# Kernel tuning notes

Hardware: AMD Instinct MI355X
Metric: run time of the kernel (lower is better)

The kernel has to match this reference:

```python
import jax, jax.numpy as jnp
import numpy as np

B, T, D, H, O = 256, 512, 128, 256, 128

def setup_inputs() -> dict:
    key = jax.random.key(0)
    ks = jax.random.split(key, 7)
    s = lambda k, shape, fan: jax.random.normal(k, shape, dtype=jnp.float32) / np.sqrt(fan)
    return {
        "x": jax.random.normal(ks[0], (B, T, D), dtype=jnp.float32),
        "W_hx_w": s(ks[1], (H, D), D),
        "W_hx_b": jnp.zeros((H,), jnp.float32),
        "W_hh_w": s(ks[2], (H, H), H),
        "W_hh_b": jnp.zeros((H,), jnp.float32),
        "W_ph_w": s(ks[3], (O, H), H),
        "W_ph_b": jnp.zeros((O,), jnp.float32),
    }

def reference(x, W_hx_w, W_hx_b, W_hh_w, W_hh_b, W_ph_w, W_ph_b):
    # Precompute the input projection for all timesteps in one batched GEMM.
    xW = jnp.einsum('btd,hd->bth', x, W_hx_w) + W_hx_b  # [B,T,H]
    h0 = jnp.zeros((x.shape[0], W_hh_w.shape[0]), x.dtype)

    def step(h, xw_t):
        h_new = jnp.tanh(xw_t + h @ W_hh_w.T + W_hh_b)
        return h_new, None

    h_T, _ = jax.lax.scan(step, h0, jnp.swapaxes(xW, 0, 1))  # scan over T
    out = h_T @ W_ph_w.T + W_ph_b  # [B,O]
    return out
```

## Files before the change

kernel.cpp:

```cpp
#include <hip/hip_runtime.h>


typedef _Float16 f16;
typedef _Float16 f16x2 __attribute__((ext_vector_type(2)));
typedef _Float16 f16x4 __attribute__((ext_vector_type(4)));
typedef _Float16 f16x8 __attribute__((ext_vector_type(8)));
typedef float f32x4 __attribute__((ext_vector_type(4)));

#define NB 256
#define NT 512
#define ND 128
#define NH 256
#define NO 128
#define R  16
#define TCH 8
#define NCH (NT / TCH)
#define STEP_F16 4096
#define WS_NEED ((size_t)16 * NT * STEP_F16 * 2)

__device__ __forceinline__ float fast_tanh(float z) {
  float e = __builtin_amdgcn_exp2f(z * 2.88539008177793f);
  float r = __builtin_amdgcn_rcpf(e + 1.0f);
  return __builtin_fmaf(-2.0f, r, 1.0f);
}

__device__ __forceinline__ f16x8 cvt8(const float* __restrict__ p) {
  f32x4 v0 = *(const f32x4*)p;
  f32x4 v1 = *(const f32x4*)(p + 4);
  f16x8 r;
  r[0] = (f16)v0.x; r[1] = (f16)v0.y; r[2] = (f16)v0.z; r[3] = (f16)v0.w;
  r[4] = (f16)v1.x; r[5] = (f16)v1.y; r[6] = (f16)v1.z; r[7] = (f16)v1.w;
  return r;
}

__device__ __forceinline__ f16x8 cvt44(const float* __restrict__ p0,
                                       const float* __restrict__ p1) {
  f32x4 a = *(const f32x4*)p0;
  f32x4 b = *(const f32x4*)p1;
  f16x8 r;
  r[0] = (f16)a.x; r[1] = (f16)a.y; r[2] = (f16)a.z; r[3] = (f16)a.w;
  r[4] = (f16)b.x; r[5] = (f16)b.y; r[6] = (f16)b.z; r[7] = (f16)b.w;
  return r;
}

__global__ __launch_bounds__(256, 2)
void xw_gemm(const float* __restrict__ x,
             const float* __restrict__ Wx, const float* __restrict__ bx,
             const float* __restrict__ bh, f16* __restrict__ ws)
{
  const int wgb = blockIdx.x & 15;
  const int c   = blockIdx.x >> 4;
  const int tid = threadIdx.x;
  const int w   = tid >> 6;
  const int l15 = tid & 15;
  const int g   = (tid >> 4) & 3;

  __shared__ alignas(16) f16 xlds[TCH * R][ND];

  f16x8 fWx[4][4];
  f32x4 bias4[4];
  #pragma unroll
  for (int ct = 0; ct < 4; ++ct) {
    const int j = w * 64 + ct * 16 + l15;
    #pragma unroll
    for (int kt = 0; kt < 4; ++kt)
      fWx[ct][kt] = cvt8(Wx + (size_t)j * ND + kt * 32 + g * 8);
    const int j0 = w * 64 + ct * 16 + g * 4;
    #pragma unroll
    for (int rg = 0; rg < 4; ++rg)
      bias4[ct][rg] = bx[j0 + rg] + bh[j0 + rg];
  }

  const int srow = tid >> 4;
  const int sq   = tid & 15;
  const float* xc = x + ((size_t)(wgb * R + srow) * NT + (size_t)c * TCH) * ND;
  #pragma unroll
  for (int jj = 0; jj < 16; ++jj) {
    const int f = (sq + jj * 16) * 4;
    f32x4 v = *(const f32x4*)(xc + f);
    const int t = f >> 7;
    const int d = f & (ND - 1);
    const int m = t * R + srow;
    f16x4 h4;
    h4[0] = (f16)v.x; h4[1] = (f16)v.y; h4[2] = (f16)v.z; h4[3] = (f16)v.w;
    *(f16x4*)((char*)&xlds[m][0] + ((2 * d) ^ ((m & 7) << 4))) = h4;
  }
  __syncthreads();

  #pragma unroll
  for (int t = 0; t < TCH; ++t) {
    f16x8 b[4];
    #pragma unroll
    for (int kt = 0; kt < 4; ++kt) {
      const int m = t * R + l15;
      b[kt] = *(const f16x8*)((char*)&xlds[m][0] +
               ((kt * 64 + g * 16) ^ ((m & 7) << 4)));
    }
    f16* wsp = ws + ((size_t)(wgb * NT + c * TCH + t)) * STEP_F16
                  + w * 1024 + g * 64 + l15 * 4;
    #pragma unroll
    for (int ct = 0; ct < 4; ++ct) {
      f32x4 ac = bias4[ct];
      #pragma unroll
      for (int kt = 0; kt < 4; ++kt)
        ac = __builtin_amdgcn_mfma_f32_16x16x32_f16(fWx[ct][kt], b[kt], ac, 0, 0, 0);
      f16x4 p;
      p[0] = (f16)ac[0]; p[1] = (f16)ac[1]; p[2] = (f16)ac[2]; p[3] = (f16)ac[3];
      *(f16x4*)(wsp + ct * 256) = p;
    }
  }
}

#define DO_STEP(CUR, ACIN, ACOUT, XWPF, XWIN, H8K, TAU)                     \
  {                                                                         \
    f16x8 bfr[7];                                                           \
    _Pragma("unroll")                                                       \
    for (int kr = 1; kr < 8; ++kr)                                          \
      bfr[kr - 1] = *(const f16x8*)((const char*)&hbuf[CUR][l15][0] +       \
                ((((w2 + kr) * 4 + g + l15) & 31) << 4));                   \
    int pf = (TAU) + 2; pf = pf < NT ? pf : NT - 1;                         \
    _Pragma("unroll")                                                       \
    for (int ct = 0; ct < 2; ++ct)                                          \
      XWPF[ct] = *(const f16x4*)(wsg + (size_t)pf * STEP_F16 + ct * 256);   \
    _Pragma("unroll")                                                       \
    for (int ct = 0; ct < 2; ++ct)                                          \
      ACIN[ct] = __builtin_amdgcn_mfma_f32_16x16x32_f16(fWh[ct][0], H8K,    \
                   ACIN[ct], 0, 0, 0);                                      \
    _Pragma("unroll")                                                       \
    for (int kr = 1; kr < 8; ++kr) {                                        \
      _Pragma("unroll")                                                     \
      for (int ct = 0; ct < 2; ++ct)                                        \
        ACIN[ct] = __builtin_amdgcn_mfma_f32_16x16x32_f16(fWh[ct][kr],      \
                     bfr[kr - 1], ACIN[ct], 0, 0, 0);                       \
    }                                                                       \
    {                                                                       \
      f16x8 h8;                                                             \
      _Pragma("unroll")                                                     \
      for (int ct = 0; ct < 2; ++ct)                                        \
        _Pragma("unroll")                                                   \
        for (int rg = 0; rg < 4; ++rg)                                      \
          h8[ct * 4 + rg] = (f16)fast_tanh(ACIN[ct][rg]);                   \
      *(f16x8*)((char*)&hbuf[(CUR) ^ 1][l15][0] +                           \
                (((w2 * 4 + g + l15) & 31) << 4)) = h8;                     \
      H8K = h8;                                                             \
    }                                                                       \
    _Pragma("unroll")                                                       \
    for (int ct = 0; ct < 2; ++ct) {                                        \
      ACOUT[ct][0] = (float)XWIN[ct][0]; ACOUT[ct][1] = (float)XWIN[ct][1]; \
      ACOUT[ct][2] = (float)XWIN[ct][2]; ACOUT[ct][3] = (float)XWIN[ct][3]; \
    }                                                                       \
    asm volatile("s_waitcnt lgkmcnt(0)\n\ts_barrier" ::: "memory");         \
    __builtin_amdgcn_sched_barrier(0);                                      \
  }

__global__ __launch_bounds__(512, 2)
void rnn_scan(const f16* __restrict__ ws,
              const float* __restrict__ Wh,
              const float* __restrict__ Wp, const float* __restrict__ bp,
              float* __restrict__ out)
{
  const int wg  = blockIdx.x;
  const int tid = threadIdx.x;
  const int w2  = tid >> 6;
  const int l15 = tid & 15;
  const int g   = (tid >> 4) & 3;

  __shared__ alignas(16) f16 hbuf[2][R][NH];

  f16x8 fWh[2][8];
  #pragma unroll
  for (int ct = 0; ct < 2; ++ct) {
    const int j = w2 * 32 + ct * 16 + l15;
    #pragma unroll
    for (int kr = 0; kr < 8; ++kr) {
      const int kta = (w2 + kr) & 7;
      fWh[ct][kr] = cvt44(Wh + (size_t)j * NH + kta * 32 + g * 4,
                          Wh + (size_t)j * NH + kta * 32 + 16 + g * 4);
    }
  }

  {
    unsigned* hz = (unsigned*)&hbuf[0][0][0];
    #pragma unroll
    for (int k = 0; k < (2 * R * NH / 2) / 512; ++k) hz[tid + k * 512] = 0u;
  }

  const f16* wsg = ws + (size_t)wg * NT * STEP_F16
                 + (size_t)(w2 * 2) * 256 + g * 64 + l15 * 4;

  f16x4 xA[2], xB[2];
  #pragma unroll
  for (int ct = 0; ct < 2; ++ct) xA[ct] = *(const f16x4*)(wsg + 0 * STEP_F16 + ct * 256);
  #pragma unroll
  for (int ct = 0; ct < 2; ++ct) xB[ct] = *(const f16x4*)(wsg + 1 * STEP_F16 + ct * 256);

  f32x4 acA[2], acB[2];
  #pragma unroll
  for (int ct = 0; ct < 2; ++ct) {
    acA[ct][0] = (float)xA[ct][0]; acA[ct][1] = (float)xA[ct][1];
    acA[ct][2] = (float)xA[ct][2]; acA[ct][3] = (float)xA[ct][3];
  }

  f16x8 h8k;
  #pragma unroll
  for (int i = 0; i < 8; ++i) h8k[i] = (f16)0.f;

  __syncthreads();

  #pragma unroll 1
  for (int tau = 0; tau < NT; tau += 2) {
    DO_STEP(0, acA, acB, xA, xB, h8k, tau);
    DO_STEP(1, acB, acA, xB, xA, h8k, tau + 1);
  }

  f16x8 bh8[8];
  #pragma unroll
  for (int kt = 0; kt < 8; ++kt)
    bh8[kt] = *(const f16x8*)((const char*)&hbuf[0][l15][0] +
              (((kt * 4 + g + l15) & 31) << 4));
  {
    const int j0 = w2 * 16 + g * 4;
    f32x4 ac = {bp[j0], bp[j0 + 1], bp[j0 + 2], bp[j0 + 3]};
    #pragma unroll
    for (int kt = 0; kt < 8; ++kt) {
      const float* wrow = Wp + (size_t)(w2 * 16 + l15) * NH;
      f16x8 afr = cvt44(wrow + kt * 32 + g * 4, wrow + kt * 32 + 16 + g * 4);
      ac = __builtin_amdgcn_mfma_f32_16x16x32_f16(afr, bh8[kt], ac, 0, 0, 0);
    }
    #pragma unroll
    for (int rg = 0; rg < 4; ++rg)
      out[(size_t)(wg * R + l15) * NO + j0 + rg] = ac[rg];
  }
}

__global__ __launch_bounds__(256, 1)
void rnn_mfma(const float* __restrict__ x,
              const float* __restrict__ Wx, const float* __restrict__ bx,
              const float* __restrict__ Wh, const float* __restrict__ bh,
              const float* __restrict__ Wp, const float* __restrict__ bp,
              float* __restrict__ out)
{
  const int wg  = blockIdx.x;
  const int tid = threadIdx.x;
  const int w   = tid >> 6;
  const int l15 = tid & 15;
  const int g   = (tid >> 4) & 3;

  __shared__ alignas(16) f16 xlds[TCH * R][ND];
  __shared__ alignas(16) f16 hbuf[2][R][NH];

  f16x8 fWh[4][8];
  #pragma unroll
  for (int ct = 0; ct < 4; ++ct) {
    const int j = w * 64 + ct * 16 + l15;
    #pragma unroll
    for (int kt = 0; kt < 8; ++kt)
      fWh[ct][kt] = cvt8(Wh + (size_t)j * NH + kt * 32 + g * 8);
  }
  f16x8 fWx[4][4];
  #pragma unroll
  for (int ct = 0; ct < 4; ++ct) {
    const int j = w * 64 + ct * 16 + l15;
    #pragma unroll
    for (int kt = 0; kt < 4; ++kt)
      fWx[ct][kt] = cvt8(Wx + (size_t)j * ND + kt * 32 + g * 8);
  }
  float bias[4];
  #pragma unroll
  for (int ct = 0; ct < 4; ++ct) {
    const int j = w * 64 + ct * 16 + l15;
    bias[ct] = bx[j] + bh[j];
  }
  {
    unsigned* hz = (unsigned*)&hbuf[0][0][0];
    #pragma unroll
    for (int k = 0; k < (R * NH / 2) / 256; ++k) hz[tid + k * 256] = 0u;
  }
  __syncthreads();

  int cur = 0;
  f16x2 xwb[TCH][4][2];
  const int srow = tid >> 4;
  const int sq   = tid & 15;
  const float* xrow = x + (size_t)(wg * R + srow) * NT * ND;

  #pragma unroll 1
  for (int c = 0; c < NCH; ++c) {
    const float* xc = xrow + (size_t)c * TCH * ND;
    #pragma unroll
    for (int jj = 0; jj < 16; ++jj) {
      const int f = (sq + jj * 16) * 4;
      f32x4 v = *(const f32x4*)(xc + f);
      const int t = f >> 7;
      const int d = f & (ND - 1);
      const int m = t * R + srow;
      f16x4 h4;
      h4[0] = (f16)v.x; h4[1] = (f16)v.y; h4[2] = (f16)v.z; h4[3] = (f16)v.w;
      *(f16x4*)((char*)&xlds[m][0] + ((2 * d) ^ ((m & 7) << 4))) = h4;
    }
    __syncthreads();

    #pragma unroll
    for (int t = 0; t < TCH; ++t) {
      f16x8 a[4];
      #pragma unroll
      for (int kt = 0; kt < 4; ++kt) {
        const int m = t * R + l15;
        a[kt] = *(const f16x8*)((char*)&xlds[m][0] +
                 ((kt * 64 + g * 16) ^ ((m & 7) << 4)));
      }
      #pragma unroll
      for (int ct = 0; ct < 4; ++ct) {
        f32x4 ac = {bias[ct], bias[ct], bias[ct], bias[ct]};
        #pragma unroll
        for (int kt = 0; kt < 4; ++kt)
          ac = __builtin_amdgcn_mfma_f32_16x16x32_f16(a[kt], fWx[ct][kt], ac, 0, 0, 0);
        f16x2 p0; p0[0] = (f16)ac[0]; p0[1] = (f16)ac[1];
        f16x2 p1; p1[0] = (f16)ac[2]; p1[1] = (f16)ac[3];
        xwb[t][ct][0] = p0;
        xwb[t][ct][1] = p1;
      }
    }

    #pragma unroll
    for (int s = 0; s < TCH; ++s) {
      f16x8 a[8];
      #pragma unroll
      for (int kt = 0; kt < 8; ++kt) {
        const int m = l15;
        a[kt] = *(const f16x8*)((char*)&hbuf[cur][m][0] +
                 ((kt * 64 + g * 16) ^ ((m & 7) << 4)));
      }
      const int nxt = cur ^ 1;
      #pragma unroll
      for (int ct = 0; ct < 4; ++ct) {
        f32x4 ac  = {(float)xwb[s][ct][0][0], (float)xwb[s][ct][0][1],
                     (float)xwb[s][ct][1][0], (float)xwb[s][ct][1][1]};
        f32x4 ac2 = {0.f, 0.f, 0.f, 0.f};
        #pragma unroll
        for (int kt = 0; kt < 4; ++kt) {
          ac  = __builtin_amdgcn_mfma_f32_16x16x32_f16(a[2*kt],     fWh[ct][2*kt],     ac,  0, 0, 0);
          ac2 = __builtin_amdgcn_mfma_f32_16x16x32_f16(a[2*kt + 1], fWh[ct][2*kt + 1], ac2, 0, 0, 0);
        }
        #pragma unroll
        for (int rg = 0; rg < 4; ++rg) {
          const float th = fast_tanh(ac[rg] + ac2[rg]);
          const int row = g * 4 + rg;
          const int col = w * 64 + ct * 16 + l15;
          *(f16*)((char*)&hbuf[nxt][row][0] +
                  ((2 * col) ^ ((row & 7) << 4))) = (f16)th;
        }
      }
      cur = nxt;
      __syncthreads();
    }
  }

  f16x8 ah[8];
  #pragma unroll
  for (int kt = 0; kt < 8; ++kt) {
    const int m = l15;
    ah[kt] = *(const f16x8*)((char*)&hbuf[cur][m][0] +
             ((kt * 64 + g * 16) ^ ((m & 7) << 4)));
  }
  #pragma unroll
  for (int ct = 0; ct < 2; ++ct) {
    const int o = w * 32 + ct * 16 + l15;
    f32x4 ac = {bp[o], bp[o], bp[o], bp[o]};
    #pragma unroll
    for (int kt = 0; kt < 8; ++kt) {
      f16x8 bfr = cvt8(Wp + (size_t)o * NH + kt * 32 + g * 8);
      ac = __builtin_amdgcn_mfma_f32_16x16x32_f16(ah[kt], bfr, ac, 0, 0, 0);
    }
    #pragma unroll
    for (int rg = 0; rg < 4; ++rg) {
      const int row = g * 4 + rg;
      out[(size_t)(wg * R + row) * NO + o] = ac[rg];
    }
  }
}

extern "C" void kernel_launch(void* const* d_in, const int* in_sizes, int n_in,
                              void* d_out, int out_size, void* d_ws, size_t ws_size,
                              hipStream_t stream) {
  const float* x   = (const float*)d_in[0];
  const float* whx = (const float*)d_in[1];
  const float* bhx = (const float*)d_in[2];
  const float* whh = (const float*)d_in[3];
  const float* bhh = (const float*)d_in[4];
  const float* wph = (const float*)d_in[5];
  const float* bph = (const float*)d_in[6];
  float* out = (float*)d_out;

  if (ws_size >= WS_NEED) {
    f16* ws = (f16*)d_ws;
    xw_gemm<<<dim3(16 * NCH), dim3(256), 0, stream>>>(x, whx, bhx, bhh, ws);
    rnn_scan<<<dim3(16), dim3(512), 0, stream>>>(ws, whh, wph, bph, out);
  } else {
    rnn_mfma<<<dim3(NB / R), dim3(256), 0, stream>>>(x, whx, bhx, whh, bhh, wph, bph, out);
  }
}
```

Baseline: 330.2 us.

## Fuse input-projection GEMM and recurrent scan into one producer/consumer kernel

Replaces the two-launch sequence (xW GEMM, then scan) with one persistent kernel. Blocks 0-15 run the recurrence, and 240 producer blocks compute the xW chunks and publish per-chunk release flags in workspace. Scan blocks spin on acquire loads before consuming each group of chunks, so the GEMM overlaps with the serial recurrence instead of running ahead of it. This adds a memset of the flags, relies on all blocks being co-resident to avoid deadlock, and the producer order must keep ahead of the consumers.

```diff
diff --git a/kernel.cpp b/kernel.cpp
--- a/kernel.cpp
+++ b/kernel.cpp
@@ -16,7 +16,10 @@
 #define TCH 8
 #define NCH (NT / TCH)
 #define STEP_F16 4096
-#define WS_NEED ((size_t)16 * NT * STEP_F16 * 2)
+#define NPROD 240
+#define NPAIR (16 * NCH)
+#define WS_XW ((size_t)16 * NT * STEP_F16 * 2)
+#define WS_FUSED (WS_XW + 4096)
 
 __device__ __forceinline__ float fast_tanh(float z) {
   float e = __builtin_amdgcn_exp2f(z * 2.88539008177793f);
@@ -41,74 +44,6 @@
   r[0] = (f16)a.x; r[1] = (f16)a.y; r[2] = (f16)a.z; r[3] = (f16)a.w;
   r[4] = (f16)b.x; r[5] = (f16)b.y; r[6] = (f16)b.z; r[7] = (f16)b.w;
   return r;
-}
-
-__global__ __launch_bounds__(256, 2)
-void xw_gemm(const float* __restrict__ x,
-             const float* __restrict__ Wx, const float* __restrict__ bx,
-             const float* __restrict__ bh, f16* __restrict__ ws)
-{
-  const int wgb = blockIdx.x & 15;
-  const int c   = blockIdx.x >> 4;
-  const int tid = threadIdx.x;
-  const int w   = tid >> 6;
-  const int l15 = tid & 15;
-  const int g   = (tid >> 4) & 3;
-
-  __shared__ alignas(16) f16 xlds[TCH * R][ND];
-
-  f16x8 fWx[4][4];
-  f32x4 bias4[4];
-  #pragma unroll
-  for (int ct = 0; ct < 4; ++ct) {
-    const int j = w * 64 + ct * 16 + l15;
-    #pragma unroll
-    for (int kt = 0; kt < 4; ++kt)
-      fWx[ct][kt] = cvt8(Wx + (size_t)j * ND + kt * 32 + g * 8);
-    const int j0 = w * 64 + ct * 16 + g * 4;
-    #pragma unroll
-    for (int rg = 0; rg < 4; ++rg)
-      bias4[ct][rg] = bx[j0 + rg] + bh[j0 + rg];
-  }
-
-  const int srow = tid >> 4;
-  const int sq   = tid & 15;
-  const float* xc = x + ((size_t)(wgb * R + srow) * NT + (size_t)c * TCH) * ND;
-  #pragma unroll
-  for (int jj = 0; jj < 16; ++jj) {
-    const int f = (sq + jj * 16) * 4;
-    f32x4 v = *(const f32x4*)(xc + f);
-    const int t = f >> 7;
-    const int d = f & (ND - 1);
-    const int m = t * R + srow;
-    f16x4 h4;
-    h4[0] = (f16)v.x; h4[1] = (f16)v.y; h4[2] = (f16)v.z; h4[3] = (f16)v.w;
-    *(f16x4*)((char*)&xlds[m][0] + ((2 * d) ^ ((m & 7) << 4))) = h4;
-  }
-  __syncthreads();
-
-  #pragma unroll
-  for (int t = 0; t < TCH; ++t) {
-    f16x8 b[4];
-    #pragma unroll
-    for (int kt = 0; kt < 4; ++kt) {
-      const int m = t * R + l15;
-      b[kt] = *(const f16x8*)((char*)&xlds[m][0] +
-               ((kt * 64 + g * 16) ^ ((m & 7) << 4)));
-    }
-    f16* wsp = ws + ((size_t)(wgb * NT + c * TCH + t)) * STEP_F16
-                  + w * 1024 + g * 64 + l15 * 4;
-    #pragma unroll
-    for (int ct = 0; ct < 4; ++ct) {
-      f32x4 ac = bias4[ct];
-      #pragma unroll
-      for (int kt = 0; kt < 4; ++kt)
-        ac = __builtin_amdgcn_mfma_f32_16x16x32_f16(fWx[ct][kt], b[kt], ac, 0, 0, 0);
-      f16x4 p;
-      p[0] = (f16)ac[0]; p[1] = (f16)ac[1]; p[2] = (f16)ac[2]; p[3] = (f16)ac[3];
-      *(f16x4*)(wsp + ct * 256) = p;
-    }
-  }
 }
 
 #define DO_STEP(CUR, ACIN, ACOUT, XWPF, XWIN, H8K, TAU)                     \
@@ -154,6 +89,245 @@
   }
 
 __global__ __launch_bounds__(512, 2)
+void rnn_fused(const float* __restrict__ x,
+               const float* __restrict__ Wx, const float* __restrict__ bx,
+               const float* __restrict__ Wh, const float* __restrict__ bh,
+               const float* __restrict__ Wp, const float* __restrict__ bp,
+               f16* __restrict__ ws, unsigned* __restrict__ flags,
+               float* __restrict__ out)
+{
+  __shared__ alignas(16) f16 smem[16384];
+  const int tid = threadIdx.x;
+  const int w2  = tid >> 6;
+  const int l15 = tid & 15;
+  const int g   = (tid >> 4) & 3;
+
+  if (blockIdx.x >= 16) {
+    f16 (*xlds)[ND] = (f16 (*)[ND])smem;
+
+    f16x8 fWx[2][4];
+    f32x4 bias2[2];
+    #pragma unroll
+    for (int ct = 0; ct < 2; ++ct) {
+      const int j = w2 * 32 + ct * 16 + l15;
+      #pragma unroll
+      for (int kt = 0; kt < 4; ++kt)
+        fWx[ct][kt] = cvt8(Wx + (size_t)j * ND + kt * 32 + g * 8);
+      const int j0 = w2 * 32 + ct * 16 + g * 4;
+      #pragma unroll
+      for (int rg = 0; rg < 4; ++rg)
+        bias2[ct][rg] = bx[j0 + rg] + bh[j0 + rg];
+    }
+
+    #pragma unroll 1
+    for (int p = blockIdx.x - 16; p < NPAIR; p += NPROD) {
+      const int s = p & 15;
+      const int c = p >> 4;
+      #pragma unroll
+      for (int jj = 0; jj < 8; ++jj) {
+        const int fi = (tid + jj * 512) * 4;
+        const int t  = fi >> 11;
+        const int rr = (fi >> 7) & 15;
+        const int d  = fi & 127;
+        f32x4 v = *(const f32x4*)(x + ((size_t)(s * R + rr) * NT
+                                     + (size_t)(c * TCH + t)) * ND + d);
+        const int m = t * R + rr;
+        f16x4 h4;
+        h4[0] = (f16)v.x; h4[1] = (f16)v.y; h4[2] = (f16)v.z; h4[3] = (f16)v.w;
+        *(f16x4*)((char*)&xlds[m][0] + ((2 * d) ^ ((m & 7) << 4))) = h4;
+      }
+      __syncthreads();
+
+      #pragma unroll
+      for (int t = 0; t < TCH; ++t) {
+        f16x8 b[4];
+        #pragma unroll
+        for (int kt = 0; kt < 4; ++kt) {
+          const int m = t * R + l15;
+          b[kt] = *(const f16x8*)((char*)&xlds[m][0] +
+                   ((kt * 64 + g * 16) ^ ((m & 7) << 4)));
+        }
+        f16* wsp = ws + ((size_t)(s * NT + c * TCH + t)) * STEP_F16
+                      + (w2 * 2) * 256 + g * 64 + l15 * 4;
+        #pragma unroll
+        for (int ct = 0; ct < 2; ++ct) {
+          f32x4 ac = bias2[ct];
+          #pragma unroll
+          for (int kt = 0; kt < 4; ++kt)
+            ac = __builtin_amdgcn_mfma_f32_16x16x32_f16(fWx[ct][kt], b[kt], ac, 0, 0, 0);
+          f16x4 pk;
+          pk[0] = (f16)ac[0]; pk[1] = (f16)ac[1];
+          pk[2] = (f16)ac[2]; pk[3] = (f16)ac[3];
+          *(f16x4*)(wsp + ct * 256) = pk;
+        }
+      }
+      __threadfence();
+      __syncthreads();
+      if (tid == 0)
+        __hip_atomic_store(&flags[p], 1u, __ATOMIC_RELEASE,
+                           __HIP_MEMORY_SCOPE_AGENT);
+    }
+    return;
+  }
+
+  const int wg = blockIdx.x;
+  f16 (*hbuf)[R][NH] = (f16 (*)[R][NH])smem;
+
+  f16x8 fWh[2][8];
+  #pragma unroll
+  for (int ct = 0; ct < 2; ++ct) {
+    const int j = w2 * 32 + ct * 16 + l15;
+    #pragma unroll
+    for (int kr = 0; kr < 8; ++kr) {
+      const int kta = (w2 + kr) & 7;
+      fWh[ct][kr] = cvt44(Wh + (size_t)j * NH + kta * 32 + g * 4,
+                          Wh + (size_t)j * NH + kta * 32 + 16 + g * 4);
+    }
+  }
+
+  {
+    unsigned* hz = (unsigned*)&hbuf[0][0][0];
+    #pragma unroll
+    for (int k = 0; k < (2 * R * NH / 2) / 512; ++k) hz[tid + k * 512] = 0u;
+  }
+
+  if (tid < 5) {
+    int cc = tid; if (cc > NCH - 1) cc = NCH - 1;
+    const int fidx = cc * 16 + wg;
+    while (__hip_atomic_load(&flags[fidx], __ATOMIC_ACQUIRE,
+                             __HIP_MEMORY_SCOPE_AGENT) == 0u)
+      __builtin_amdgcn_s_sleep(8);
+  }
+  __syncthreads();
+
+  const f16* wsg = ws + (size_t)wg * NT * STEP_F16
+                 + (size_t)(w2 * 2) * 256 + g * 64 + l15 * 4;
+
+  f16x4 xA[2], xB[2];
+  #pragma unroll
+  for (int ct = 0; ct < 2; ++ct) xA[ct] = *(const f16x4*)(wsg + 0 * STEP_F16 + ct * 256);
+  #pragma unroll
+  for (int ct = 0; ct < 2; ++ct) xB[ct] = *(const f16x4*)(wsg + 1 * STEP_F16 + ct * 256);
+
+  f32x4 acA[2], acB[2];
+  #pragma unroll
+  for (int ct = 0; ct < 2; ++ct) {
+    acA[ct][0] = (float)xA[ct][0]; acA[ct][1] = (float)xA[ct][1];
+    acA[ct][2] = (float)xA[ct][2]; acA[ct][3] = (float)xA[ct][3];
+  }
+
+  f16x8 h8k;
+  #pragma unroll
+  for (int i = 0; i < 8; ++i) h8k[i] = (f16)0.f;
+
+  #pragma unroll 1
+  for (int c4 = 0; c4 < NCH; c4 += 4) {
+    if (c4 > 0) {
+      if (tid < 4) {
+        int cc = c4 + 1 + tid; if (cc > NCH - 1) cc = NCH - 1;
+        const int fidx = cc * 16 + wg;
+        while (__hip_atomic_load(&flags[fidx], __ATOMIC_ACQUIRE,
+                                 __HIP_MEMORY_SCOPE_AGENT) == 0u)
+          __builtin_amdgcn_s_sleep(8);
+      }
+      __syncthreads();
+    }
+    #pragma unroll 1
+    for (int tau = c4 * 8; tau < c4 * 8 + 32; tau += 2) {
+      DO_STEP(0, acA, acB, xA, xB, h8k, tau);
+      DO_STEP(1, acB, acA, xB, xA, h8k, tau + 1);
+    }
+  }
+
+  f16x8 bh8[8];
+  #pragma unroll
+  for (int kt = 0; kt < 8; ++kt)
+    bh8[kt] = *(const f16x8*)((const char*)&hbuf[0][l15][0] +
+              (((kt * 4 + g + l15) & 31) << 4));
+  {
+    const int j0 = w2 * 16 + g * 4;
+    f32x4 ac = {bp[j0], bp[j0 + 1], bp[j0 + 2], bp[j0 + 3]};
+    #pragma unroll
+    for (int kt = 0; kt < 8; ++kt) {
+      const float* wrow = Wp + (size_t)(w2 * 16 + l15) * NH;
+      f16x8 afr = cvt44(wrow + kt * 32 + g * 4, wrow + kt * 32 + 16 + g * 4);
+      ac = __builtin_amdgcn_mfma_f32_16x16x32_f16(afr, bh8[kt], ac, 0, 0, 0);
+    }
+    #pragma unroll
+    for (int rg = 0; rg < 4; ++rg)
+      out[(size_t)(wg * R + l15) * NO + j0 + rg] = ac[rg];
+  }
+}
+
+__global__ __launch_bounds__(256, 2)
+void xw_gemm(const float* __restrict__ x,
+             const float* __restrict__ Wx, const float* __restrict__ bx,
+             const float* __restrict__ bh, f16* __restrict__ ws)
+{
+  const int wgb = blockIdx.x & 15;
+  const int c   = blockIdx.x >> 4;
+  const int tid = threadIdx.x;
+  const int w   = tid >> 6;
+  const int l15 = tid & 15;
+  const int g   = (tid >> 4) & 3;
+
+  __shared__ alignas(16) f16 xlds[TCH * R][ND];
+
+  f16x8 fWx[4][4];
+  f32x4 bias4[4];
+  #pragma unroll
+  for (int ct = 0; ct < 4; ++ct) {
+    const int j = w * 64 + ct * 16 + l15;
+    #pragma unroll
+    for (int kt = 0; kt < 4; ++kt)
+      fWx[ct][kt] = cvt8(Wx + (size_t)j * ND + kt * 32 + g * 8);
+    const int j0 = w * 64 + ct * 16 + g * 4;
+    #pragma unroll
+    for (int rg = 0; rg < 4; ++rg)
+      bias4[ct][rg] = bx[j0 + rg] + bh[j0 + rg];
+  }
+
+  const int srow = tid >> 4;
+  const int sq   = tid & 15;
+  const float* xc = x + ((size_t)(wgb * R + srow) * NT + (size_t)c * TCH) * ND;
+  #pragma unroll
+  for (int jj = 0; jj < 16; ++jj) {
+    const int f = (sq + jj * 16) * 4;
+    f32x4 v = *(const f32x4*)(xc + f);
+    const int t = f >> 7;
+    const int d = f & (ND - 1);
+    const int m = t * R + srow;
+    f16x4 h4;
+    h4[0] = (f16)v.x; h4[1] = (f16)v.y; h4[2] = (f16)v.z; h4[3] = (f16)v.w;
+    *(f16x4*)((char*)&xlds[m][0] + ((2 * d) ^ ((m & 7) << 4))) = h4;
+  }
+  __syncthreads();
+
+  #pragma unroll
+  for (int t = 0; t < TCH; ++t) {
+    f16x8 b[4];
+    #pragma unroll
+    for (int kt = 0; kt < 4; ++kt) {
+      const int m = t * R + l15;
+      b[kt] = *(const f16x8*)((char*)&xlds[m][0] +
+               ((kt * 64 + g * 16) ^ ((m & 7) << 4)));
+    }
+    f16* wsp = ws + ((size_t)(wgb * NT + c * TCH + t)) * STEP_F16
+                  + w * 1024 + g * 64 + l15 * 4;
+    #pragma unroll
+    for (int ct = 0; ct < 4; ++ct) {
+      f32x4 ac = bias4[ct];
+      #pragma unroll
+      for (int kt = 0; kt < 4; ++kt)
+        ac = __builtin_amdgcn_mfma_f32_16x16x32_f16(fWx[ct][kt], b[kt], ac, 0, 0, 0);
+      f16x4 p;
+      p[0] = (f16)ac[0]; p[1] = (f16)ac[1]; p[2] = (f16)ac[2]; p[3] = (f16)ac[3];
+      *(f16x4*)(wsp + ct * 256) = p;
+    }
+  }
+}
+
+__global__ __launch_bounds__(512, 2)
 void rnn_scan(const f16* __restrict__ ws,
               const float* __restrict__ Wh,
               const float* __restrict__ Wp, const float* __restrict__ bp,
@@ -230,153 +404,6 @@
     #pragma unroll
     for (int rg = 0; rg < 4; ++rg)
       out[(size_t)(wg * R + l15) * NO + j0 + rg] = ac[rg];
-  }
-}
-
-__global__ __launch_bounds__(256, 1)
-void rnn_mfma(const float* __restrict__ x,
-              const float* __restrict__ Wx, const float* __restrict__ bx,
-              const float* __restrict__ Wh, const float* __restrict__ bh,
-              const float* __restrict__ Wp, const float* __restrict__ bp,
-              float* __restrict__ out)
-{
-  const int wg  = blockIdx.x;
-  const int tid = threadIdx.x;
-  const int w   = tid >> 6;
-  const int l15 = tid & 15;
-  const int g   = (tid >> 4) & 3;
-
-  __shared__ alignas(16) f16 xlds[TCH * R][ND];
-  __shared__ alignas(16) f16 hbuf[2][R][NH];
-
-  f16x8 fWh[4][8];
-  #pragma unroll
-  for (int ct = 0; ct < 4; ++ct) {
-    const int j = w * 64 + ct * 16 + l15;
-    #pragma unroll
-    for (int kt = 0; kt < 8; ++kt)
-      fWh[ct][kt] = cvt8(Wh + (size_t)j * NH + kt * 32 + g * 8);
-  }
-  f16x8 fWx[4][4];
-  #pragma unroll
-  for (int ct = 0; ct < 4; ++ct) {
-    const int j = w * 64 + ct * 16 + l15;
-    #pragma unroll
-    for (int kt = 0; kt < 4; ++kt)
-      fWx[ct][kt] = cvt8(Wx + (size_t)j * ND + kt * 32 + g * 8);
-  }
-  float bias[4];
-  #pragma unroll
-  for (int ct = 0; ct < 4; ++ct) {
-    const int j = w * 64 + ct * 16 + l15;
-    bias[ct] = bx[j] + bh[j];
-  }
-  {
-    unsigned* hz = (unsigned*)&hbuf[0][0][0];
-    #pragma unroll
-    for (int k = 0; k < (R * NH / 2) / 256; ++k) hz[tid + k * 256] = 0u;
-  }
-  __syncthreads();
-
-  int cur = 0;
-  f16x2 xwb[TCH][4][2];
-  const int srow = tid >> 4;
-  const int sq   = tid & 15;
-  const float* xrow = x + (size_t)(wg * R + srow) * NT * ND;
-
-  #pragma unroll 1
-  for (int c = 0; c < NCH; ++c) {
-    const float* xc = xrow + (size_t)c * TCH * ND;
-    #pragma unroll
-    for (int jj = 0; jj < 16; ++jj) {
-      const int f = (sq + jj * 16) * 4;
-      f32x4 v = *(const f32x4*)(xc + f);
-      const int t = f >> 7;
-      const int d = f & (ND - 1);
-      const int m = t * R + srow;
-      f16x4 h4;
-      h4[0] = (f16)v.x; h4[1] = (f16)v.y; h4[2] = (f16)v.z; h4[3] = (f16)v.w;
-      *(f16x4*)((char*)&xlds[m][0] + ((2 * d) ^ ((m & 7) << 4))) = h4;
-    }
-    __syncthreads();
-
-    #pragma unroll
-    for (int t = 0; t < TCH; ++t) {
-      f16x8 a[4];
-      #pragma unroll
-      for (int kt = 0; kt < 4; ++kt) {
-        const int m = t * R + l15;
-        a[kt] = *(const f16x8*)((char*)&xlds[m][0] +
-                 ((kt * 64 + g * 16) ^ ((m & 7) << 4)));
-      }
-      #pragma unroll
-      for (int ct = 0; ct < 4; ++ct) {
-        f32x4 ac = {bias[ct], bias[ct], bias[ct], bias[ct]};
-        #pragma unroll
-        for (int kt = 0; kt < 4; ++kt)
-          ac = __builtin_amdgcn_mfma_f32_16x16x32_f16(a[kt], fWx[ct][kt], ac, 0, 0, 0);
-        f16x2 p0; p0[0] = (f16)ac[0]; p0[1] = (f16)ac[1];
-        f16x2 p1; p1[0] = (f16)ac[2]; p1[1] = (f16)ac[3];
-        xwb[t][ct][0] = p0;
-        xwb[t][ct][1] = p1;
-      }
-    }
-
-    #pragma unroll
-    for (int s = 0; s < TCH; ++s) {
-      f16x8 a[8];
-      #pragma unroll
-      for (int kt = 0; kt < 8; ++kt) {
-        const int m = l15;
-        a[kt] = *(const f16x8*)((char*)&hbuf[cur][m][0] +
-                 ((kt * 64 + g * 16) ^ ((m & 7) << 4)));
-      }
-      const int nxt = cur ^ 1;
-      #pragma unroll
-      for (int ct = 0; ct < 4; ++ct) {
-        f32x4 ac  = {(float)xwb[s][ct][0][0], (float)xwb[s][ct][0][1],
-                     (float)xwb[s][ct][1][0], (float)xwb[s][ct][1][1]};
-        f32x4 ac2 = {0.f, 0.f, 0.f, 0.f};
-        #pragma unroll
-        for (int kt = 0; kt < 4; ++kt) {
-          ac  = __builtin_amdgcn_mfma_f32_16x16x32_f16(a[2*kt],     fWh[ct][2*kt],     ac,  0, 0, 0);
-          ac2 = __builtin_amdgcn_mfma_f32_16x16x32_f16(a[2*kt + 1], fWh[ct][2*kt + 1], ac2, 0, 0, 0);
-        }
-        #pragma unroll
-        for (int rg = 0; rg < 4; ++rg) {
-          const float th = fast_tanh(ac[rg] + ac2[rg]);
-          const int row = g * 4 + rg;
-          const int col = w * 64 + ct * 16 + l15;
-          *(f16*)((char*)&hbuf[nxt][row][0] +
-                  ((2 * col) ^ ((row & 7) << 4))) = (f16)th;
-        }
-      }
-      cur = nxt;
-      __syncthreads();
-    }
-  }
-
-  f16x8 ah[8];
-  #pragma unroll
-  for (int kt = 0; kt < 8; ++kt) {
-    const int m = l15;
-    ah[kt] = *(const f16x8*)((char*)&hbuf[cur][m][0] +
-             ((kt * 64 + g * 16) ^ ((m & 7) << 4)));
-  }
-  #pragma unroll
-  for (int ct = 0; ct < 2; ++ct) {
-    const int o = w * 32 + ct * 16 + l15;
-    f32x4 ac = {bp[o], bp[o], bp[o], bp[o]};
-    #pragma unroll
-    for (int kt = 0; kt < 8; ++kt) {
-      f16x8 bfr = cvt8(Wp + (size_t)o * NH + kt * 32 + g * 8);
-      ac = __builtin_amdgcn_mfma_f32_16x16x32_f16(ah[kt], bfr, ac, 0, 0, 0);
-    }
-    #pragma unroll
-    for (int rg = 0; rg < 4; ++rg) {
-      const int row = g * 4 + rg;
-      out[(size_t)(wg * R + row) * NO + o] = ac[rg];
-    }
   }
 }
 
@@ -391,12 +418,15 @@
   const float* wph = (const float*)d_in[5];
   const float* bph = (const float*)d_in[6];
   float* out = (float*)d_out;
-
-  if (ws_size >= WS_NEED) {
-    f16* ws = (f16*)d_ws;
+  f16* ws = (f16*)d_ws;
+
+  if (ws_size >= WS_FUSED) {
+    unsigned* flags = (unsigned*)((char*)d_ws + WS_XW);
+    hipMemsetAsync(flags, 0, 4096, stream);
+    rnn_fused<<<dim3(16 + NPROD), dim3(512), 0, stream>>>(
+        x, whx, bhx, whh, bhh, wph, bph, ws, flags, out);
+  } else {
     xw_gemm<<<dim3(16 * NCH), dim3(256), 0, stream>>>(x, whx, bhx, bhh, ws);
     rnn_scan<<<dim3(16), dim3(512), 0, stream>>>(ws, whh, wph, bph, out);
-  } else {
-    rnn_mfma<<<dim3(NB / R), dim3(256), 0, stream>>>(x, whx, bhx, whh, bhh, wph, bph, out);
-  }
-}
+  }
+}
```

Result: slower. 520.2 us (+57.5%).
